# Kernel optimization log

Hardware: AMD Instinct MI355X
Metric: run time of the kernel (lower is better)

Reference implementation:

```python
import jax, jax.numpy as jnp
import numpy as np

B, C, H, W = 16, 64, 128, 128
K = 3  # dynamic kernel size


def setup_inputs() -> dict:
    key = jax.random.key(0)
    ks = jax.random.split(key, 6)
    return {
        "x": jax.random.normal(ks[0], (B, C, H, W), jnp.float32),       # feature map
        "d": jax.random.normal(ks[1], (B, 64), jnp.float32),            # degradation repr
        "Wk1": jax.random.normal(ks[2], (64, 64), jnp.float32) * 0.05,  # Linear(64,64), no bias
        "Wk2": jax.random.normal(ks[3], (64 * K * K, 64), jnp.float32) * 0.05,  # Linear(64,576)
        "Wc": jax.random.normal(ks[4], (64, 64), jnp.float32) * 0.05,   # 1x1 conv weight (out,in)
        "bc": jnp.zeros((64,), jnp.float32),                            # 1x1 conv bias
    }


def _lrelu(v):
    return jnp.where(v >= 0, v, 0.1 * v)


def reference(x, d, Wk1, Wk2, Wc, bc):
    b, c, h, w = x.shape
    k = K
    # kernel-generating MLP: Linear -> LeakyReLU(0.1) -> Linear
    hid = _lrelu(d @ Wk1.T)                      # (B, 64)
    kern = (hid @ Wk2.T).reshape(b, c, 1, k, k)   # one 3x3 kernel per (batch, channel)

    # dynamic depthwise 3x3 conv: per-sample kernels, groups == channels
    def dwconv(xi, ki):
        # xi: (C,H,W), ki: (C,1,3,3) in OIHW with feature_group_count=C
        return jax.lax.conv_general_dilated(
            xi[None], ki, window_strides=(1, 1), padding='SAME',
            feature_group_count=c,
            dimension_numbers=('NCHW', 'OIHW', 'NCHW'))[0]

    out = jax.vmap(dwconv)(x, kern)              # (B,C,H,W)
    out = _lrelu(out)
    # 1x1 pointwise conv with bias
    out = jnp.einsum('bchw,oc->bohw', out, Wc) + bc[None, :, None, None]
    return out
```

## Files before the change

kernel.cpp:

```cpp
#include <hip/hip_runtime.h>

#define Bn 16
#define Cn 64
#define Hn 128
#define Wn 128
#define HWn (Hn * Wn)

typedef __attribute__((ext_vector_type(8)))  short  short8;
typedef __attribute__((ext_vector_type(16))) float  floatx16;
typedef __attribute__((ext_vector_type(4)))  float  floatx4;
using int32x4 = int __attribute__((ext_vector_type(4)));

__device__ float
llvm_amdgcn_raw_buffer_load_fp32(int32x4 srsrc, int voffset, int soffset,
                                 int aux) __asm("llvm.amdgcn.raw.buffer.load.f32");
__device__ floatx4
llvm_amdgcn_raw_buffer_load_v4f32(int32x4 srsrc, int voffset, int soffset,
                                  int aux) __asm("llvm.amdgcn.raw.buffer.load.v4f32");

__device__ __forceinline__ int32x4 make_rsrc(const void* p, int bytes) {
    int32x4 r;
    r.x = (int)(unsigned)(uintptr_t)p;
    r.y = (int)((uintptr_t)p >> 32);
    r.z = bytes;
    r.w = 0x00020000;
    return r;
}

__device__ __forceinline__ unsigned short f2bf(float f) {
    unsigned u = __float_as_uint(f);
    u += 0x7fffu + ((u >> 16) & 1u);
    return (unsigned short)(u >> 16);
}
__device__ __forceinline__ float lrelu(float v) { return v >= 0.f ? v : 0.1f * v; }

__global__ __launch_bounds__(192)
void gen_kern6(const float* __restrict__ d,
               const float* __restrict__ Wk1,
               const float* __restrict__ Wk2,
               const float* __restrict__ Wc,
               float* __restrict__ kernP,
               unsigned short* __restrict__ WcBF) {
    const int b = blockIdx.x;
    const int r = blockIdx.y;
    const int t = threadIdx.x;
    __shared__ float hid_s[64];

    if (t < 64) {
        const float4* __restrict__ w4 = (const float4*)(Wk1 + (size_t)t * 64);
        const float*  __restrict__ db = d + b * 64;
        float s0 = 0.f, s1 = 0.f, s2 = 0.f, s3 = 0.f;
        #pragma unroll
        for (int j = 0; j < 16; ++j) {
            const float4 wv = w4[j];
            s0 += db[4 * j + 0] * wv.x;
            s1 += db[4 * j + 1] * wv.y;
            s2 += db[4 * j + 2] * wv.z;
            s3 += db[4 * j + 3] * wv.w;
        }
        hid_s[t] = lrelu((s0 + s1) + (s2 + s3));
    }
    __syncthreads();

    {
        const int o = r * 192 + t;
        const float4* __restrict__ w4 = (const float4*)(Wk2 + (size_t)o * 64);
        const float4* __restrict__ h4 = (const float4*)hid_s;
        float s0 = 0.f, s1 = 0.f, s2 = 0.f, s3 = 0.f;
        #pragma unroll
        for (int j = 0; j < 16; ++j) {
            const float4 wv = w4[j];
            const float4 hv = h4[j];
            s0 += hv.x * wv.x;
            s1 += hv.y * wv.y;
            s2 += hv.z * wv.z;
            s3 += hv.w * wv.w;
        }
        const int c = o / 9, tap = o - c * 9;
        kernP[b * 768 + c * 12 + tap] = (s0 + s1) + (s2 + s3);
    }

    if (b == 0 && r == 0) {
        for (int idx = t; idx < 4096; idx += 192)
            WcBF[idx] = f2bf(Wc[idx]);
    }
}

__global__ __launch_bounds__(256)
void da_mfma2(const float* __restrict__ x,
              const float* __restrict__ kernP,
              const unsigned short* __restrict__ WcBF,
              const float* __restrict__ bc,
              float* __restrict__ out) {
    const int t    = threadIdx.x;
    const int lane = t & 63;
    const int wv   = t >> 6;
    const int col  = lane & 31;
    const int kh   = lane >> 5;
    const int bx   = blockIdx.x;
    const int h    = ((bx & 7) << 4) | (bx >> 3);
    const int b    = blockIdx.y;

    __shared__ float tl[16 * 3 * 136];

    int rofsB[3];
    #pragma unroll
    for (int i = 0; i < 3; ++i) {
        const int hh = h + i - 1;
        rofsB[i] = (hh >= 0 && hh < Hn) ? hh * (Wn * 4) : 0x10000000;
    }

    const int32x4 rs = make_rsrc(x + (size_t)b * Cn * HWn, Cn * HWn * 4);

    floatx16 acc[2];
    #pragma unroll
    for (int m = 0; m < 2; ++m)
        #pragma unroll
        for (int r = 0; r < 16; ++r)
            acc[m][r] = bc[m * 32 + (r & 3) + 8 * (r >> 2) + 4 * kh];

    const int sch = t >> 4;
    const int px0 = (t & 15) * 8;
    const float* __restrict__ kp = kernP + b * 768;

    const int px = wv * 32 + col;

    for (int g = 0; g < 4; ++g) {
        const int c = g * 16 + sch;
        const floatx4* k4 = (const floatx4*)(kp + c * 12);
        const floatx4 k0 = k4[0];
        const floatx4 k1 = k4[1];
        const float   k8 = ((const float*)k4)[8];

        float xa[3][8];
        #pragma unroll
        for (int r = 0; r < 3; ++r) {
            const int vo = (c << 16) + rofsB[r] + px0 * 4;
            const floatx4 va = llvm_amdgcn_raw_buffer_load_v4f32(rs, vo, 0, 0);
            const floatx4 vb = llvm_amdgcn_raw_buffer_load_v4f32(rs, vo + 16, 0, 0);
            xa[r][0] = va.x; xa[r][1] = va.y; xa[r][2] = va.z; xa[r][3] = va.w;
            xa[r][4] = vb.x; xa[r][5] = vb.y; xa[r][6] = vb.z; xa[r][7] = vb.w;
        }

        float t0[8], t1[8], t2[8];
        #pragma unroll
        for (int i = 0; i < 8; ++i) {
            t0[i] = k0.x * xa[0][i] + k0.w * xa[1][i] + k1.z * xa[2][i];
            t1[i] = k0.y * xa[0][i] + k1.x * xa[1][i] + k1.w * xa[2][i];
            t2[i] = k0.z * xa[0][i] + k1.y * xa[1][i] + k8   * xa[2][i];
        }
        {
            const int base = (sch * 3) * 136 + 4 + px0;
            *(float4*)&tl[base]             = make_float4(t0[0], t0[1], t0[2], t0[3]);
            *(float4*)&tl[base + 4]         = make_float4(t0[4], t0[5], t0[6], t0[7]);
            *(float4*)&tl[base + 136]       = make_float4(t1[0], t1[1], t1[2], t1[3]);
            *(float4*)&tl[base + 140]       = make_float4(t1[4], t1[5], t1[6], t1[7]);
            *(float4*)&tl[base + 272]       = make_float4(t2[0], t2[1], t2[2], t2[3]);
            *(float4*)&tl[base + 276]       = make_float4(t2[4], t2[5], t2[6], t2[7]);
        }
        if (t < 96) {
            const int ch = t / 6, rem = t - ch * 6;
            const int dx = rem >> 1, side = rem & 1;
            tl[(ch * 3 + dx) * 136 + (side ? 132 : 3)] = 0.f;
        }
        __syncthreads();

        short8 bfr;
        #pragma unroll
        for (int j = 0; j < 8; ++j) {
            const int cl = kh * 8 + j;
            const int base = (cl * 3) * 136 + 4 + px;
            const float dw = tl[base - 1]
                           + tl[base + 136]
                           + tl[base + 273];
            bfr[j] = (short)f2bf(lrelu(dw));
        }
        const short8 a0 = *(const short8*)(WcBF + (0 * 32 + col) * 64 + g * 16 + kh * 8);
        const short8 a1 = *(const short8*)(WcBF + (1 * 32 + col) * 64 + g * 16 + kh * 8);
        acc[0] = __builtin_amdgcn_mfma_f32_32x32x16_bf16(a0, bfr, acc[0], 0, 0, 0);
        acc[1] = __builtin_amdgcn_mfma_f32_32x32x16_bf16(a1, bfr, acc[1], 0, 0, 0);
        __syncthreads();
    }

    float* __restrict__ ob = out + (size_t)b * Cn * HWn + h * Wn + px;
    #pragma unroll
    for (int m = 0; m < 2; ++m)
        #pragma unroll
        for (int r = 0; r < 16; ++r) {
            const int o = m * 32 + (r & 3) + 8 * (r >> 2) + 4 * kh;
            ob[(size_t)o * HWn] = acc[m][r];
        }
}

extern "C" void kernel_launch(void* const* d_in, const int* in_sizes, int n_in,
                              void* d_out, int out_size, void* d_ws, size_t ws_size,
                              hipStream_t stream) {
    const float* x   = (const float*)d_in[0];
    const float* d   = (const float*)d_in[1];
    const float* Wk1 = (const float*)d_in[2];
    const float* Wk2 = (const float*)d_in[3];
    const float* Wc  = (const float*)d_in[4];
    const float* bc  = (const float*)d_in[5];
    float* out = (float*)d_out;
    float*          kernP = (float*)d_ws;
    unsigned short* WcBF  = (unsigned short*)((float*)d_ws + Bn * 768);

    gen_kern6<<<dim3(Bn, 3), dim3(192), 0, stream>>>(d, Wk1, Wk2, Wc, kernP, WcBF);
    da_mfma2<<<dim3(Hn, Bn), dim3(256), 0, stream>>>(x, kernP, WcBF, bc, out);
}
```

Measured before the change: 135.6 us.

## Pipeline x loads with double-buffered bf16 depthwise tile and shuffle halos

Restructures the fused depthwise+pointwise kernel. The horizontal 3-tap reduction now happens in registers, with halo values exchanged by lane shuffles, and only the finished bf16 depthwise activations go to a small double-buffered, XOR-swizzled shared tile. The next channel group's global loads are issued before the current group's MFMAs, and one barrier per iteration replaces two. This cuts LDS traffic and barriers and overlaps memory latency with compute, at the cost of more registers for the prefetched row data.

Measured after the change: 137.1 us. Within noise of the previous version (+1.1%).

```diff
diff --git a/kernel.cpp b/kernel.cpp
--- a/kernel.cpp
+++ b/kernel.cpp
@@ -86,8 +86,54 @@
     }
 }
 
+struct XK { floatx4 x[3][2]; };
+
+__device__ __forceinline__ void issue_x(XK& v, int32x4 rs, int c,
+                                        const int* rofsB, int px0) {
+    #pragma unroll
+    for (int r = 0; r < 3; ++r) {
+        const int vo = (c << 16) + rofsB[r] + px0 * 4;
+        v.x[r][0] = llvm_amdgcn_raw_buffer_load_v4f32(rs, vo, 0, 0);
+        v.x[r][1] = llvm_amdgcn_raw_buffer_load_v4f32(rs, vo + 16, 0, 0);
+    }
+}
+
+__device__ __forceinline__ short8 compute_dw(const XK& v, const float* kp,
+                                             int c, int lane, int tm) {
+    const floatx4* k4 = (const floatx4*)(kp + c * 12);
+    const floatx4 k0 = k4[0];
+    const floatx4 k1 = k4[1];
+    const float   k8 = ((const float*)k4)[8];
+
+    float t0[8], t1[8], t2[8];
+    #pragma unroll
+    for (int i = 0; i < 8; ++i) {
+        const float xr0 = (i < 4) ? v.x[0][0][i] : v.x[0][1][i - 4];
+        const float xr1 = (i < 4) ? v.x[1][0][i] : v.x[1][1][i - 4];
+        const float xr2 = (i < 4) ? v.x[2][0][i] : v.x[2][1][i - 4];
+        t0[i] = k0.x * xr0 + k0.w * xr1 + k1.z * xr2;
+        t1[i] = k0.y * xr0 + k1.x * xr1 + k1.w * xr2;
+        t2[i] = k0.z * xr0 + k1.y * xr1 + k8   * xr2;
+    }
+    float t0m = __shfl(t0[7], lane - 1, 64);
+    float t2p = __shfl(t2[0], lane + 1, 64);
+    if (tm == 0)  t0m = 0.f;
+    if (tm == 15) t2p = 0.f;
+
+    float dw[8];
+    dw[0] = t0m + t1[0] + t2[1];
+    #pragma unroll
+    for (int i = 1; i < 7; ++i) dw[i] = t0[i - 1] + t1[i] + t2[i + 1];
+    dw[7] = t0[6] + t1[7] + t2p;
+
+    short8 w8;
+    #pragma unroll
+    for (int i = 0; i < 8; ++i) w8[i] = (short)f2bf(lrelu(dw[i]));
+    return w8;
+}
+
 __global__ __launch_bounds__(256)
-void da_mfma2(const float* __restrict__ x,
+void da_mfma3(const float* __restrict__ x,
               const float* __restrict__ kernP,
               const unsigned short* __restrict__ WcBF,
               const float* __restrict__ bc,
@@ -100,8 +146,13 @@
     const int bx   = blockIdx.x;
     const int h    = ((bx & 7) << 4) | (bx >> 3);
     const int b    = blockIdx.y;
-
-    __shared__ float tl[16 * 3 * 136];
+    const int px   = wv * 32 + col;
+
+    const int sch = t >> 4;
+    const int tm  = t & 15;
+    const int px0 = tm * 8;
+
+    __shared__ unsigned short dwB[2][2048];
 
     int rofsB[3];
     #pragma unroll
@@ -111,6 +162,7 @@
     }
 
     const int32x4 rs = make_rsrc(x + (size_t)b * Cn * HWn, Cn * HWn * 4);
+    const float* __restrict__ kp = kernP + b * 768;
 
     floatx16 acc[2];
     #pragma unroll
@@ -119,67 +171,36 @@
         for (int r = 0; r < 16; ++r)
             acc[m][r] = bc[m * 32 + (r & 3) + 8 * (r >> 2) + 4 * kh];
 
-    const int sch = t >> 4;
-    const int px0 = (t & 15) * 8;
-    const float* __restrict__ kp = kernP + b * 768;
-
-    const int px = wv * 32 + col;
-
+    {
+        XK cur;
+        issue_x(cur, rs, sch, rofsB, px0);
+        const short8 w8 = compute_dw(cur, kp, sch, lane, tm);
+        *(short8*)&dwB[0][sch * 128 + (px0 ^ ((sch & 8) << 2))] = w8;
+    }
+    __syncthreads();
+
+    #pragma unroll
     for (int g = 0; g < 4; ++g) {
-        const int c = g * 16 + sch;
-        const floatx4* k4 = (const floatx4*)(kp + c * 12);
-        const floatx4 k0 = k4[0];
-        const floatx4 k1 = k4[1];
-        const float   k8 = ((const float*)k4)[8];
-
-        float xa[3][8];
-        #pragma unroll
-        for (int r = 0; r < 3; ++r) {
-            const int vo = (c << 16) + rofsB[r] + px0 * 4;
-            const floatx4 va = llvm_amdgcn_raw_buffer_load_v4f32(rs, vo, 0, 0);
-            const floatx4 vb = llvm_amdgcn_raw_buffer_load_v4f32(rs, vo + 16, 0, 0);
-            xa[r][0] = va.x; xa[r][1] = va.y; xa[r][2] = va.z; xa[r][3] = va.w;
-            xa[r][4] = vb.x; xa[r][5] = vb.y; xa[r][6] = vb.z; xa[r][7] = vb.w;
-        }
-
-        float t0[8], t1[8], t2[8];
-        #pragma unroll
-        for (int i = 0; i < 8; ++i) {
-            t0[i] = k0.x * xa[0][i] + k0.w * xa[1][i] + k1.z * xa[2][i];
-            t1[i] = k0.y * xa[0][i] + k1.x * xa[1][i] + k1.w * xa[2][i];
-            t2[i] = k0.z * xa[0][i] + k1.y * xa[1][i] + k8   * xa[2][i];
-        }
-        {
-            const int base = (sch * 3) * 136 + 4 + px0;
-            *(float4*)&tl[base]             = make_float4(t0[0], t0[1], t0[2], t0[3]);
-            *(float4*)&tl[base + 4]         = make_float4(t0[4], t0[5], t0[6], t0[7]);
-            *(float4*)&tl[base + 136]       = make_float4(t1[0], t1[1], t1[2], t1[3]);
-            *(float4*)&tl[base + 140]       = make_float4(t1[4], t1[5], t1[6], t1[7]);
-            *(float4*)&tl[base + 272]       = make_float4(t2[0], t2[1], t2[2], t2[3]);
-            *(float4*)&tl[base + 276]       = make_float4(t2[4], t2[5], t2[6], t2[7]);
-        }
-        if (t < 96) {
-            const int ch = t / 6, rem = t - ch * 6;
-            const int dx = rem >> 1, side = rem & 1;
-            tl[(ch * 3 + dx) * 136 + (side ? 132 : 3)] = 0.f;
-        }
-        __syncthreads();
+        XK nxt;
+        if (g < 3)
+            issue_x(nxt, rs, (g + 1) * 16 + sch, rofsB, px0);
 
         short8 bfr;
         #pragma unroll
         for (int j = 0; j < 8; ++j) {
             const int cl = kh * 8 + j;
-            const int base = (cl * 3) * 136 + 4 + px;
-            const float dw = tl[base - 1]
-                           + tl[base + 136]
-                           + tl[base + 273];
-            bfr[j] = (short)f2bf(lrelu(dw));
+            bfr[j] = (short)dwB[g & 1][cl * 128 + (px ^ ((cl & 8) << 2))];
         }
         const short8 a0 = *(const short8*)(WcBF + (0 * 32 + col) * 64 + g * 16 + kh * 8);
         const short8 a1 = *(const short8*)(WcBF + (1 * 32 + col) * 64 + g * 16 + kh * 8);
         acc[0] = __builtin_amdgcn_mfma_f32_32x32x16_bf16(a0, bfr, acc[0], 0, 0, 0);
         acc[1] = __builtin_amdgcn_mfma_f32_32x32x16_bf16(a1, bfr, acc[1], 0, 0, 0);
-        __syncthreads();
+
+        if (g < 3) {
+            const short8 w8 = compute_dw(nxt, kp, (g + 1) * 16 + sch, lane, tm);
+            *(short8*)&dwB[(g + 1) & 1][sch * 128 + (px0 ^ ((sch & 8) << 2))] = w8;
+            __syncthreads();
+        }
     }
 
     float* __restrict__ ob = out + (size_t)b * Cn * HWn + h * Wn + px;
@@ -206,5 +227,5 @@
     unsigned short* WcBF  = (unsigned short*)((float*)d_ws + Bn * 768);
 
     gen_kern6<<<dim3(Bn, 3), dim3(192), 0, stream>>>(d, Wk1, Wk2, Wc, kernP, WcBF);
-    da_mfma2<<<dim3(Hn, Bn), dim3(256), 0, stream>>>(x, kernP, WcBF, bc, out);
-}
+    da_mfma3<<<dim3(Hn, Bn), dim3(256), 0, stream>>>(x, kernP, WcBF, bc, out);
+}
```
